# Kernel optimization log

Measured on AMD Instinct MI355X. Metric: run time of the kernel, lower is better.

## Reference

```python
import jax, jax.numpy as jnp
import numpy as np

N = 50000   # nodes
E = 800000  # edges (avg degree 16)
D = 128     # hidden dim (GNN_hidden_dim), heads=1
SLOPE = 0.2  # LeakyReLU negative slope (PyG default)


def _w(k, shape, fan_in):
    return jax.random.normal(k, shape, dtype=jnp.float32) * (1.0 / np.sqrt(fan_in))


def setup_inputs() -> dict:
    key = jax.random.key(0)
    ks = jax.random.split(key, 24)
    inp = {}
    inp["x"] = jax.random.normal(ks[0], (N, D), dtype=jnp.float32)
    inp["edge_index"] = jax.random.randint(ks[1], (2, E), 0, N, dtype=jnp.int32)
    # layer 1 (GATv2 + linear skip)
    inp["Wl1"] = _w(ks[2], (D, D), D); inp["Wr1"] = _w(ks[3], (D, D), D)
    inp["att1"] = _w(ks[4], (D,), D); inp["b1"] = jnp.zeros((D,), jnp.float32)
    inp["Wlin1"] = _w(ks[5], (D, D), D); inp["blin1"] = jnp.zeros((D,), jnp.float32)
    # layer 2
    inp["Wl2"] = _w(ks[6], (D, D), D); inp["Wr2"] = _w(ks[7], (D, D), D)
    inp["att2"] = _w(ks[8], (D,), D); inp["b2"] = jnp.zeros((D,), jnp.float32)
    inp["Wlin2"] = _w(ks[9], (D, D), D); inp["blin2"] = jnp.zeros((D,), jnp.float32)
    # output layer (out_channels=1, heads=1)
    inp["Wlo"] = _w(ks[10], (D, 1), D); inp["Wro"] = _w(ks[11], (D, 1), D)
    inp["atto"] = _w(ks[12], (1,), 1); inp["bo"] = jnp.zeros((1,), jnp.float32)
    inp["Wlino"] = _w(ks[13], (D, 1), D); inp["blino"] = jnp.zeros((1,), jnp.float32)
    return inp


def gatv2(x, src, dst, Wl, Wr, att, b):
    # GATv2 (PyG, add_self_loops=False, share_weights=False, heads=1, no edge_attr)
    xl = x @ Wl            # [N, C] source transform (also message content)
    xr = x @ Wr            # [N, C] target transform
    e = jax.nn.leaky_relu(xl[src] + xr[dst], SLOPE) @ att  # [E] edge logits
    m = jax.ops.segment_max(e, dst, num_segments=N)
    m = jnp.where(jnp.isfinite(m), m, 0.0)  # empty segments
    p = jnp.exp(e - m[dst])
    s = jax.ops.segment_sum(p, dst, num_segments=N)
    alpha = p / (s[dst] + 1e-16)            # segment softmax over incoming edges
    out = jax.ops.segment_sum(alpha[:, None] * xl[src], dst, num_segments=N)
    return out + b


def reference(x, edge_index, Wl1, Wr1, att1, b1, Wlin1, blin1,
              Wl2, Wr2, att2, b2, Wlin2, blin2,
              Wlo, Wro, atto, bo, Wlino, blino):
    src, dst = edge_index[0], edge_index[1]
    h = jax.nn.relu(gatv2(x, src, dst, Wl1, Wr1, att1, b1) + x @ Wlin1 + blin1)
    h = jax.nn.relu(gatv2(h, src, dst, Wl2, Wr2, att2, b2) + h @ Wlin2 + blin2)
    out = gatv2(h, src, dst, Wlo, Wro, atto, bo) + h @ Wlino + blino
    return out  # [N, 1]
```

## Files before the change

kernel.cpp:

```cpp
#include <hip/hip_runtime.h>
#include <hip/hip_bf16.h>
#include <math.h>

#define NN 50000
#define EE 800000
#define DD 128
#define SLOPE 0.2f

typedef __attribute__((ext_vector_type(8))) short short8;
typedef __attribute__((ext_vector_type(4))) float f32x4;

static __device__ __forceinline__ float wred_sum(float v) {
#pragma unroll
    for (int m = 1; m < 64; m <<= 1) v += __shfl_xor(v, m, 64);
    return v;
}

static __device__ __forceinline__ ushort f2bf(float f) {
    __hip_bfloat16 b = __float2bfloat16(f);
    return *reinterpret_cast<ushort*>(&b);
}
static __device__ __forceinline__ float bf2f(unsigned int u) {
    return __uint_as_float((u & 0xffffu) << 16);
}
static __device__ __forceinline__ void unpack8(const uint4& xp, float* xv) {
    xv[0] = bf2f(xp.x); xv[1] = bf2f(xp.x >> 16);
    xv[2] = bf2f(xp.y); xv[3] = bf2f(xp.y >> 16);
    xv[4] = bf2f(xp.z); xv[5] = bf2f(xp.z >> 16);
    xv[6] = bf2f(xp.w); xv[7] = bf2f(xp.w >> 16);
}

__global__ void k_degree(const int* __restrict__ dstv, int* __restrict__ deg,
                         int* __restrict__ epos) {
    int i = blockIdx.x * blockDim.x + threadIdx.x;
    if (i < EE) epos[i] = atomicAdd(&deg[dstv[i]], 1);
}

__global__ void k_blocksum(const int* __restrict__ deg, int* __restrict__ bsum) {
    int t = threadIdx.x;
    int idx = blockIdx.x * 256 + t;
    int v = (idx < NN) ? deg[idx] : 0;
#pragma unroll
    for (int m = 1; m < 64; m <<= 1) v += __shfl_xor(v, m, 64);
    __shared__ int part[4];
    if ((t & 63) == 0) part[t >> 6] = v;
    __syncthreads();
    if (t == 0) bsum[blockIdx.x] = part[0] + part[1] + part[2] + part[3];
}

__global__ void k_scan_bsum(const int* __restrict__ bsum, int* __restrict__ boff, int nb) {
    __shared__ int sd[2][256];
    int t = threadIdx.x;
    int v = (t < nb) ? bsum[t] : 0;
    sd[0][t] = v;
    __syncthreads();
    int s = 0;
    for (int off = 1; off < 256; off <<= 1) {
        int x = sd[s][t];
        if (t >= off) x += sd[s][t - off];
        sd[s ^ 1][t] = x;
        s ^= 1;
        __syncthreads();
    }
    if (t < nb) boff[t] = sd[s][t] - v;
}

__global__ void k_scan_final(const int* __restrict__ deg, const int* __restrict__ boff,
                             int* __restrict__ offs) {
    __shared__ int sd[2][256];
    int t = threadIdx.x;
    int idx = blockIdx.x * 256 + t;
    int v = (idx < NN) ? deg[idx] : 0;
    sd[0][t] = v;
    __syncthreads();
    int s = 0;
    for (int off = 1; off < 256; off <<= 1) {
        int x = sd[s][t];
        if (t >= off) x += sd[s][t - off];
        sd[s ^ 1][t] = x;
        s ^= 1;
        __syncthreads();
    }
    int incl = sd[s][t];
    int base = boff[blockIdx.x];
    if (idx < NN) offs[idx + 1] = base + incl;
    if (idx == 0) offs[0] = 0;
}

__global__ void k_scatter(const int* __restrict__ srcv, const int* __restrict__ dstv,
                          const int* __restrict__ offs, const int* __restrict__ epos,
                          int* __restrict__ csr_src) {
    int i = blockIdx.x * blockDim.x + threadIdx.x;
    if (i < EE) csr_src[offs[dstv[i]] + epos[i]] = srcv[i];
}

__global__ __launch_bounds__(256) void k_wconvert(
    const float* __restrict__ W0, const float* __restrict__ W1, const float* __restrict__ W2,
    const float* __restrict__ W3, const float* __restrict__ W4, const float* __restrict__ W5,
    ushort* __restrict__ Wt) {
    int idx = blockIdx.x * 256 + threadIdx.x;
    int i = idx >> 14;
    int r = idx & 16383;
    int n = r >> 7;
    int k = r & 127;
    const float* Ws[6] = {W0, W1, W2, W3, W4, W5};
    Wt[idx] = f2bf(Ws[i][k * DD + n]);
}

template <int XBF>
__global__ __launch_bounds__(256) void k_gemm3m(
    const float* __restrict__ Xf,
    const ushort* __restrict__ Xb,
    const ushort* __restrict__ Wt,
    ushort* __restrict__ O0b,
    float* __restrict__ O1,
    float* __restrict__ O2) {
    __shared__ ushort wsh[128 * 136];
    int t = threadIdx.x;
    int wid = t >> 6, lane = t & 63;
    int m0 = blockIdx.x * 128 + wid * 32;
    int qrow = lane & 15, kg = lane >> 4;

    short8 afrag[2][4];
#pragma unroll
    for (int mg = 0; mg < 2; mg++) {
#pragma unroll
        for (int ks = 0; ks < 4; ks++) {
            int row = m0 + mg * 16 + qrow;
            row = (row < NN) ? row : (NN - 1);
            if (XBF) {
                afrag[mg][ks] = *reinterpret_cast<const short8*>(
                    Xb + (size_t)row * DD + ks * 32 + kg * 8);
            } else {
                const float* p = Xf + (size_t)row * DD + ks * 32 + kg * 8;
                float4 u0 = *reinterpret_cast<const float4*>(p);
                float4 u1 = *reinterpret_cast<const float4*>(p + 4);
                short8 s;
                s[0] = (short)f2bf(u0.x); s[1] = (short)f2bf(u0.y);
                s[2] = (short)f2bf(u0.z); s[3] = (short)f2bf(u0.w);
                s[4] = (short)f2bf(u1.x); s[5] = (short)f2bf(u1.y);
                s[6] = (short)f2bf(u1.z); s[7] = (short)f2bf(u1.w);
                afrag[mg][ks] = s;
            }
        }
    }

    for (int w = 0; w < 3; w++) {
        __syncthreads();
        const ushort* Wb = Wt + (size_t)w * DD * DD;
#pragma unroll
        for (int i = 0; i < 8; i++) {
            int flat = i * 256 + t;
            int row = flat >> 4, ch = flat & 15;
            short8 v = *reinterpret_cast<const short8*>(Wb + row * DD + ch * 8);
            *reinterpret_cast<short8*>(&wsh[row * 136 + ch * 8]) = v;
        }
        __syncthreads();

        f32x4 acc[2][8];
#pragma unroll
        for (int mg = 0; mg < 2; mg++)
#pragma unroll
            for (int ng = 0; ng < 8; ng++) acc[mg][ng] = (f32x4)(0.f);

#pragma unroll
        for (int ks = 0; ks < 4; ks++) {
            short8 bfrag[8];
#pragma unroll
            for (int ng = 0; ng < 8; ng++)
                bfrag[ng] = *reinterpret_cast<const short8*>(
                    &wsh[(ng * 16 + qrow) * 136 + ks * 32 + kg * 8]);
#pragma unroll
            for (int mg = 0; mg < 2; mg++)
#pragma unroll
                for (int ng = 0; ng < 8; ng++)
                    acc[mg][ng] = __builtin_amdgcn_mfma_f32_16x16x32_bf16(
                        afrag[mg][ks], bfrag[ng], acc[mg][ng], 0, 0, 0);
        }

#pragma unroll
        for (int mg = 0; mg < 2; mg++) {
#pragma unroll
            for (int r = 0; r < 4; r++) {
                int row = m0 + mg * 16 + kg * 4 + r;
                if (row < NN) {
#pragma unroll
                    for (int ng = 0; ng < 8; ng++) {
                        int col = ng * 16 + qrow;
                        float v = acc[mg][ng][r];
                        if (w == 0) O0b[(size_t)row * DD + col] = f2bf(v);
                        else if (w == 1) O1[(size_t)row * DD + col] = v;
                        else O2[(size_t)row * DD + col] = v;
                    }
                }
            }
        }
    }
}

template <int OUTVEC>
__global__ __launch_bounds__(256, 8) void k_fused(
    const int* __restrict__ offs, const int* __restrict__ csr_src,
    const ushort* __restrict__ xlb,
    const float* __restrict__ xr,
    const float* __restrict__ att,
    const float* __restrict__ lin, const float* __restrict__ bb,
    const float* __restrict__ blin, ushort* __restrict__ houtb,
    const float* __restrict__ Wlo, const float* __restrict__ Wro,
    const float* __restrict__ Wlino, const float* __restrict__ blino,
    float* __restrict__ xlo, float* __restrict__ xro, float* __restrict__ lino,
    int nwaves) {
    int gwave = (blockIdx.x * blockDim.x + threadIdx.x) >> 6;
    int lane = threadIdx.x & 63;
    int q = lane >> 4;
    int ql = lane & 15;
    int c0 = ql * 8;

    float av[8];
    {
        float4 a0 = *reinterpret_cast<const float4*>(att + c0);
        float4 a1 = *reinterpret_cast<const float4*>(att + c0 + 4);
        av[0] = a0.x; av[1] = a0.y; av[2] = a0.z; av[3] = a0.w;
        av[4] = a1.x; av[5] = a1.y; av[6] = a1.z; av[7] = a1.w;
    }

    for (int wid = gwave; wid < NN; wid += nwaves) {
        int start = offs[wid];
        int deg = offs[wid + 1] - start;

        float xrv[8];
        {
            float4 t0 = *reinterpret_cast<const float4*>(xr + (size_t)wid * DD + c0);
            float4 t1 = *reinterpret_cast<const float4*>(xr + (size_t)wid * DD + c0 + 4);
            xrv[0] = t0.x; xrv[1] = t0.y; xrv[2] = t0.z; xrv[3] = t0.w;
            xrv[4] = t1.x; xrv[5] = t1.y; xrv[6] = t1.z; xrv[7] = t1.w;
        }

        float ss = 0.f;
        float acc[8];
#pragma unroll
        for (int c = 0; c < 8; c++) acc[c] = 0.f;

        int s_cur = (q < deg) ? csr_src[start + q] : 0;
        uint4 xp = *reinterpret_cast<const uint4*>(xlb + (size_t)s_cur * DD + c0);
        for (int j = q; j < deg; j += 4) {
            int jn = j + 4;
            int s_nxt = (jn < deg) ? csr_src[start + jn] : 0;
            uint4 xpn = *reinterpret_cast<const uint4*>(xlb + (size_t)s_nxt * DD + c0);
            float xv[8];
            unpack8(xp, xv);
            float v = 0.f;
#pragma unroll
            for (int c = 0; c < 8; c++) {
                float u = xv[c] + xrv[c];
                v += fmaxf(u, SLOPE * u) * av[c];
            }
#pragma unroll
            for (int msk = 1; msk < 16; msk <<= 1) v += __shfl_xor(v, msk, 64);
            float p = __expf(v);
            ss += p;
#pragma unroll
            for (int c = 0; c < 8; c++) acc[c] += p * xv[c];
            xp = xpn;
        }

#pragma unroll
        for (int msk = 16; msk < 64; msk <<= 1) {
            ss += __shfl_xor(ss, msk, 64);
#pragma unroll
            for (int c = 0; c < 8; c++) acc[c] += __shfl_xor(acc[c], msk, 64);
        }

        if (q == 0) {
            float inv = 1.f / (ss + 1e-16f);
            float4 l0 = *reinterpret_cast<const float4*>(lin + (size_t)wid * DD + c0);
            float4 l1 = *reinterpret_cast<const float4*>(lin + (size_t)wid * DD + c0 + 4);
            float4 b0 = *reinterpret_cast<const float4*>(bb + c0);
            float4 b1 = *reinterpret_cast<const float4*>(bb + c0 + 4);
            float4 bl0 = *reinterpret_cast<const float4*>(blin + c0);
            float4 bl1 = *reinterpret_cast<const float4*>(blin + c0 + 4);
            float lv[8] = {l0.x, l0.y, l0.z, l0.w, l1.x, l1.y, l1.z, l1.w};
            float bv[8] = {b0.x, b0.y, b0.z, b0.w, b1.x, b1.y, b1.z, b1.w};
            float blv[8] = {bl0.x, bl0.y, bl0.z, bl0.w, bl1.x, bl1.y, bl1.z, bl1.w};
            float o[8];
#pragma unroll
            for (int c = 0; c < 8; c++) o[c] = fmaxf(acc[c] * inv + bv[c] + lv[c] + blv[c], 0.f);

            if (!OUTVEC) {
                uint4 pk;
                pk.x = (unsigned)f2bf(o[0]) | ((unsigned)f2bf(o[1]) << 16);
                pk.y = (unsigned)f2bf(o[2]) | ((unsigned)f2bf(o[3]) << 16);
                pk.z = (unsigned)f2bf(o[4]) | ((unsigned)f2bf(o[5]) << 16);
                pk.w = (unsigned)f2bf(o[6]) | ((unsigned)f2bf(o[7]) << 16);
                *reinterpret_cast<uint4*>(houtb + (size_t)wid * DD + c0) = pk;
            } else {
                float4 w0a = *reinterpret_cast<const float4*>(Wlo + c0);
                float4 w0b = *reinterpret_cast<const float4*>(Wlo + c0 + 4);
                float4 w1a = *reinterpret_cast<const float4*>(Wro + c0);
                float4 w1b = *reinterpret_cast<const float4*>(Wro + c0 + 4);
                float4 w2a = *reinterpret_cast<const float4*>(Wlino + c0);
                float4 w2b = *reinterpret_cast<const float4*>(Wlino + c0 + 4);
                float wv0[8] = {w0a.x, w0a.y, w0a.z, w0a.w, w0b.x, w0b.y, w0b.z, w0b.w};
                float wv1[8] = {w1a.x, w1a.y, w1a.z, w1a.w, w1b.x, w1b.y, w1b.z, w1b.w};
                float wv2[8] = {w2a.x, w2a.y, w2a.z, w2a.w, w2b.x, w2b.y, w2b.z, w2b.w};
                float d0 = 0.f, d1 = 0.f, d2 = 0.f;
#pragma unroll
                for (int c = 0; c < 8; c++) {
                    d0 += o[c] * wv0[c];
                    d1 += o[c] * wv1[c];
                    d2 += o[c] * wv2[c];
                }
#pragma unroll
                for (int msk = 1; msk < 16; msk <<= 1) {
                    d0 += __shfl_xor(d0, msk, 64);
                    d1 += __shfl_xor(d1, msk, 64);
                    d2 += __shfl_xor(d2, msk, 64);
                }
                if (ql == 0) {
                    xlo[wid] = d0;
                    xro[wid] = d1;
                    lino[wid] = d2 + blino[0];
                }
            }
        }
    }
}

__global__ __launch_bounds__(256) void k_aggout(
    const int* __restrict__ offs, const int* __restrict__ csr_src,
    const float* __restrict__ xlo, const float* __restrict__ xro,
    const float* __restrict__ atto, const float* __restrict__ lino,
    const float* __restrict__ bo, float* __restrict__ out) {
    int wid = (blockIdx.x * blockDim.x + threadIdx.x) >> 6;
    int lane = threadIdx.x & 63;
    if (wid >= NN) return;
    int start = offs[wid];
    int deg = offs[wid + 1] - start;
    float xro_w = xro[wid];
    float a0 = atto[0];

    float sl = 0.f, nl = 0.f;
    for (int j = lane; j < deg; j += 64) {
        int s = csr_src[start + j];
        float xs = xlo[s];
        float u = xs + xro_w;
        float e = fmaxf(u, SLOPE * u) * a0;
        float p = __expf(e);
        sl += p;
        nl += p * xs;
    }
    sl = wred_sum(sl);
    nl = wred_sum(nl);
    if (lane == 0) out[wid] = nl / (sl + 1e-16f) + bo[0] + lino[wid];
}

extern "C" void kernel_launch(void* const* d_in, const int* in_sizes, int n_in,
                              void* d_out, int out_size, void* d_ws, size_t ws_size,
                              hipStream_t stream) {
    const float* x = (const float*)d_in[0];
    const int* ei = (const int*)d_in[1];
    const int* srcv = ei;
    const int* dstv = ei + EE;
    const float* Wl1 = (const float*)d_in[2];
    const float* Wr1 = (const float*)d_in[3];
    const float* att1 = (const float*)d_in[4];
    const float* b1 = (const float*)d_in[5];
    const float* Wlin1 = (const float*)d_in[6];
    const float* blin1 = (const float*)d_in[7];
    const float* Wl2 = (const float*)d_in[8];
    const float* Wr2 = (const float*)d_in[9];
    const float* att2 = (const float*)d_in[10];
    const float* b2 = (const float*)d_in[11];
    const float* Wlin2 = (const float*)d_in[12];
    const float* blin2 = (const float*)d_in[13];
    const float* Wlo = (const float*)d_in[14];
    const float* Wro = (const float*)d_in[15];
    const float* atto = (const float*)d_in[16];
    const float* bo = (const float*)d_in[17];
    const float* Wlino = (const float*)d_in[18];
    const float* blino = (const float*)d_in[19];

    char* w = (char*)d_ws;
    auto alloc = [&](size_t bytes) {
        void* p = (void*)w;
        w += (bytes + 255) & ~(size_t)255;
        return p;
    };
    ushort* xlb = (ushort*)alloc((size_t)NN * DD * 2);
    float* xr = (float*)alloc((size_t)NN * DD * 4);
    float* lin = (float*)alloc((size_t)NN * DD * 4);
    ushort* hb = (ushort*)alloc((size_t)NN * DD * 2);
    ushort* Wt = (ushort*)alloc((size_t)6 * DD * DD * 2);
    float* xlo = (float*)alloc((size_t)NN * 4);
    float* xro = (float*)alloc((size_t)NN * 4);
    float* lino = (float*)alloc((size_t)NN * 4);
    int* deg = (int*)alloc((size_t)NN * 4);
    int* offs = (int*)alloc((size_t)(NN + 1) * 4);
    int* bsum = (int*)alloc(256 * 4);
    int* boff = (int*)alloc(256 * 4);
    int* csr_src = (int*)alloc((size_t)(EE + 8) * 4);
    int* epos = (int*)alloc((size_t)EE * 4);

    const int NB = (NN + 255) / 256;

    hipMemsetAsync(deg, 0, (size_t)NN * 4, stream);
    k_degree<<<(EE + 255) / 256, 256, 0, stream>>>(dstv, deg, epos);
    k_blocksum<<<NB, 256, 0, stream>>>(deg, bsum);
    k_scan_bsum<<<1, 256, 0, stream>>>(bsum, boff, NB);
    k_scan_final<<<NB, 256, 0, stream>>>(deg, boff, offs);
    k_scatter<<<(EE + 255) / 256, 256, 0, stream>>>(srcv, dstv, offs, epos, csr_src);

    k_wconvert<<<(6 * DD * DD) / 256, 256, 0, stream>>>(Wl1, Wr1, Wlin1, Wl2, Wr2, Wlin2, Wt);

    const int GEMM_GRID = (NN + 127) / 128;
    const int NODE_GRID = (NN * 64 + 255) / 256;
    const int PERS_BLOCKS = 2048;
    const int PERS_WAVES = PERS_BLOCKS * 4;

    k_gemm3m<0><<<GEMM_GRID, 256, 0, stream>>>(x, nullptr, Wt + (size_t)0 * 3 * DD * DD,
                                               xlb, xr, lin);
    k_fused<0><<<PERS_BLOCKS, 256, 0, stream>>>(offs, csr_src, xlb, xr, att1, lin, b1, blin1, hb,
                                                nullptr, nullptr, nullptr, nullptr,
                                                nullptr, nullptr, nullptr, PERS_WAVES);
    k_gemm3m<1><<<GEMM_GRID, 256, 0, stream>>>(nullptr, hb, Wt + (size_t)1 * 3 * DD * DD,
                                               xlb, xr, lin);
    k_fused<1><<<PERS_BLOCKS, 256, 0, stream>>>(offs, csr_src, xlb, xr, att2, lin, b2, blin2,
                                                nullptr, Wlo, Wro, Wlino, blino,
                                                xlo, xro, lino, PERS_WAVES);
    k_aggout<<<NODE_GRID, 256, 0, stream>>>(offs, csr_src, xlo, xro, atto, lino, bo, (float*)d_out);
}
```

Before: 220.2 us.

## Store xr and skip projections in bf16 and use one wave per node

The GEMM now writes all three projections (xl, xr, linear skip) as bf16 instead of writing xr and lin in fp32, which halves the bytes written and later read for those buffers. The fused aggregation kernel drops the persistent grid-stride loop and the software prefetch of the next neighbour row. It launches one wave per node with default launch bounds instead. The aim is to cut memory traffic and let the hardware scheduler hide gather latency, at the cost of some precision in xr and the skip term and the loss of explicit prefetching.

Result: no change. 223.2 us (+1.4%).

```diff
diff --git a/kernel.cpp b/kernel.cpp
--- a/kernel.cpp
+++ b/kernel.cpp
@@ -113,8 +113,8 @@
     const ushort* __restrict__ Xb,
     const ushort* __restrict__ Wt,
     ushort* __restrict__ O0b,
-    float* __restrict__ O1,
-    float* __restrict__ O2) {
+    ushort* __restrict__ O1b,
+    ushort* __restrict__ O2b) {
     __shared__ ushort wsh[128 * 136];
     int t = threadIdx.x;
     int wid = t >> 6, lane = t & 63;
@@ -178,6 +178,7 @@
                         afrag[mg][ks], bfrag[ng], acc[mg][ng], 0, 0, 0);
         }
 
+        ushort* Ob = (w == 0) ? O0b : (w == 1) ? O1b : O2b;
 #pragma unroll
         for (int mg = 0; mg < 2; mg++) {
 #pragma unroll
@@ -187,10 +188,7 @@
 #pragma unroll
                     for (int ng = 0; ng < 8; ng++) {
                         int col = ng * 16 + qrow;
-                        float v = acc[mg][ng][r];
-                        if (w == 0) O0b[(size_t)row * DD + col] = f2bf(v);
-                        else if (w == 1) O1[(size_t)row * DD + col] = v;
-                        else O2[(size_t)row * DD + col] = v;
+                        Ob[(size_t)row * DD + col] = f2bf(acc[mg][ng][r]);
                     }
                 }
             }
@@ -199,19 +197,20 @@
 }
 
 template <int OUTVEC>
-__global__ __launch_bounds__(256, 8) void k_fused(
+__global__ __launch_bounds__(256) void k_fused(
     const int* __restrict__ offs, const int* __restrict__ csr_src,
     const ushort* __restrict__ xlb,
-    const float* __restrict__ xr,
+    const ushort* __restrict__ xrb,
     const float* __restrict__ att,
-    const float* __restrict__ lin, const float* __restrict__ bb,
+    const ushort* __restrict__ linb,
+    const float* __restrict__ bb,
     const float* __restrict__ blin, ushort* __restrict__ houtb,
     const float* __restrict__ Wlo, const float* __restrict__ Wro,
     const float* __restrict__ Wlino, const float* __restrict__ blino,
-    float* __restrict__ xlo, float* __restrict__ xro, float* __restrict__ lino,
-    int nwaves) {
-    int gwave = (blockIdx.x * blockDim.x + threadIdx.x) >> 6;
+    float* __restrict__ xlo, float* __restrict__ xro, float* __restrict__ lino) {
+    int wid = (blockIdx.x * blockDim.x + threadIdx.x) >> 6;
     int lane = threadIdx.x & 63;
+    if (wid >= NN) return;
     int q = lane >> 4;
     int ql = lane & 15;
     int c0 = ql * 8;
@@ -223,104 +222,97 @@
         av[0] = a0.x; av[1] = a0.y; av[2] = a0.z; av[3] = a0.w;
         av[4] = a1.x; av[5] = a1.y; av[6] = a1.z; av[7] = a1.w;
     }
-
-    for (int wid = gwave; wid < NN; wid += nwaves) {
-        int start = offs[wid];
-        int deg = offs[wid + 1] - start;
-
-        float xrv[8];
+    float xrv[8];
+    {
+        uint4 xrp = *reinterpret_cast<const uint4*>(xrb + (size_t)wid * DD + c0);
+        unpack8(xrp, xrv);
+    }
+
+    int start = offs[wid];
+    int deg = offs[wid + 1] - start;
+
+    float ss = 0.f;
+    float acc[8];
+#pragma unroll
+    for (int c = 0; c < 8; c++) acc[c] = 0.f;
+
+    for (int j = q; j < deg; j += 4) {
+        int s = csr_src[start + j];
+        uint4 xp = *reinterpret_cast<const uint4*>(xlb + (size_t)s * DD + c0);
+        float xv[8];
+        unpack8(xp, xv);
+        float v = 0.f;
+#pragma unroll
+        for (int c = 0; c < 8; c++) {
+            float u = xv[c] + xrv[c];
+            v += fmaxf(u, SLOPE * u) * av[c];
+        }
+#pragma unroll
+        for (int msk = 1; msk < 16; msk <<= 1) v += __shfl_xor(v, msk, 64);
+        float p = __expf(v);
+        ss += p;
+#pragma unroll
+        for (int c = 0; c < 8; c++) acc[c] += p * xv[c];
+    }
+
+#pragma unroll
+    for (int msk = 16; msk < 64; msk <<= 1) {
+        ss += __shfl_xor(ss, msk, 64);
+#pragma unroll
+        for (int c = 0; c < 8; c++) acc[c] += __shfl_xor(acc[c], msk, 64);
+    }
+
+    if (q == 0) {
+        float inv = 1.f / (ss + 1e-16f);
+        float lv[8];
         {
-            float4 t0 = *reinterpret_cast<const float4*>(xr + (size_t)wid * DD + c0);
-            float4 t1 = *reinterpret_cast<const float4*>(xr + (size_t)wid * DD + c0 + 4);
-            xrv[0] = t0.x; xrv[1] = t0.y; xrv[2] = t0.z; xrv[3] = t0.w;
-            xrv[4] = t1.x; xrv[5] = t1.y; xrv[6] = t1.z; xrv[7] = t1.w;
-        }
-
-        float ss = 0.f;
-        float acc[8];
-#pragma unroll
-        for (int c = 0; c < 8; c++) acc[c] = 0.f;
-
-        int s_cur = (q < deg) ? csr_src[start + q] : 0;
-        uint4 xp = *reinterpret_cast<const uint4*>(xlb + (size_t)s_cur * DD + c0);
-        for (int j = q; j < deg; j += 4) {
-            int jn = j + 4;
-            int s_nxt = (jn < deg) ? csr_src[start + jn] : 0;
-            uint4 xpn = *reinterpret_cast<const uint4*>(xlb + (size_t)s_nxt * DD + c0);
-            float xv[8];
-            unpack8(xp, xv);
-            float v = 0.f;
+            uint4 lp = *reinterpret_cast<const uint4*>(linb + (size_t)wid * DD + c0);
+            unpack8(lp, lv);
+        }
+        float4 b0 = *reinterpret_cast<const float4*>(bb + c0);
+        float4 b1 = *reinterpret_cast<const float4*>(bb + c0 + 4);
+        float4 bl0 = *reinterpret_cast<const float4*>(blin + c0);
+        float4 bl1 = *reinterpret_cast<const float4*>(blin + c0 + 4);
+        float bv[8] = {b0.x, b0.y, b0.z, b0.w, b1.x, b1.y, b1.z, b1.w};
+        float blv[8] = {bl0.x, bl0.y, bl0.z, bl0.w, bl1.x, bl1.y, bl1.z, bl1.w};
+        float o[8];
+#pragma unroll
+        for (int c = 0; c < 8; c++) o[c] = fmaxf(acc[c] * inv + bv[c] + lv[c] + blv[c], 0.f);
+
+        if (!OUTVEC) {
+            uint4 pk;
+            pk.x = (unsigned)f2bf(o[0]) | ((unsigned)f2bf(o[1]) << 16);
+            pk.y = (unsigned)f2bf(o[2]) | ((unsigned)f2bf(o[3]) << 16);
+            pk.z = (unsigned)f2bf(o[4]) | ((unsigned)f2bf(o[5]) << 16);
+            pk.w = (unsigned)f2bf(o[6]) | ((unsigned)f2bf(o[7]) << 16);
+            *reinterpret_cast<uint4*>(houtb + (size_t)wid * DD + c0) = pk;
+        } else {
+            float4 w0a = *reinterpret_cast<const float4*>(Wlo + c0);
+            float4 w0b = *reinterpret_cast<const float4*>(Wlo + c0 + 4);
+            float4 w1a = *reinterpret_cast<const float4*>(Wro + c0);
+            float4 w1b = *reinterpret_cast<const float4*>(Wro + c0 + 4);
+            float4 w2a = *reinterpret_cast<const float4*>(Wlino + c0);
+            float4 w2b = *reinterpret_cast<const float4*>(Wlino + c0 + 4);
+            float wv0[8] = {w0a.x, w0a.y, w0a.z, w0a.w, w0b.x, w0b.y, w0b.z, w0b.w};
+            float wv1[8] = {w1a.x, w1a.y, w1a.z, w1a.w, w1b.x, w1b.y, w1b.z, w1b.w};
+            float wv2[8] = {w2a.x, w2a.y, w2a.z, w2a.w, w2b.x, w2b.y, w2b.z, w2b.w};
+            float d0 = 0.f, d1 = 0.f, d2 = 0.f;
 #pragma unroll
             for (int c = 0; c < 8; c++) {
-                float u = xv[c] + xrv[c];
-                v += fmaxf(u, SLOPE * u) * av[c];
+                d0 += o[c] * wv0[c];
+                d1 += o[c] * wv1[c];
+                d2 += o[c] * wv2[c];
             }
 #pragma unroll
-            for (int msk = 1; msk < 16; msk <<= 1) v += __shfl_xor(v, msk, 64);
-            float p = __expf(v);
-            ss += p;
-#pragma unroll
-            for (int c = 0; c < 8; c++) acc[c] += p * xv[c];
-            xp = xpn;
-        }
-
-#pragma unroll
-        for (int msk = 16; msk < 64; msk <<= 1) {
-            ss += __shfl_xor(ss, msk, 64);
-#pragma unroll
-            for (int c = 0; c < 8; c++) acc[c] += __shfl_xor(acc[c], msk, 64);
-        }
-
-        if (q == 0) {
-            float inv = 1.f / (ss + 1e-16f);
-            float4 l0 = *reinterpret_cast<const float4*>(lin + (size_t)wid * DD + c0);
-            float4 l1 = *reinterpret_cast<const float4*>(lin + (size_t)wid * DD + c0 + 4);
-            float4 b0 = *reinterpret_cast<const float4*>(bb + c0);
-            float4 b1 = *reinterpret_cast<const float4*>(bb + c0 + 4);
-            float4 bl0 = *reinterpret_cast<const float4*>(blin + c0);
-            float4 bl1 = *reinterpret_cast<const float4*>(blin + c0 + 4);
-            float lv[8] = {l0.x, l0.y, l0.z, l0.w, l1.x, l1.y, l1.z, l1.w};
-            float bv[8] = {b0.x, b0.y, b0.z, b0.w, b1.x, b1.y, b1.z, b1.w};
-            float blv[8] = {bl0.x, bl0.y, bl0.z, bl0.w, bl1.x, bl1.y, bl1.z, bl1.w};
-            float o[8];
-#pragma unroll
-            for (int c = 0; c < 8; c++) o[c] = fmaxf(acc[c] * inv + bv[c] + lv[c] + blv[c], 0.f);
-
-            if (!OUTVEC) {
-                uint4 pk;
-                pk.x = (unsigned)f2bf(o[0]) | ((unsigned)f2bf(o[1]) << 16);
-                pk.y = (unsigned)f2bf(o[2]) | ((unsigned)f2bf(o[3]) << 16);
-                pk.z = (unsigned)f2bf(o[4]) | ((unsigned)f2bf(o[5]) << 16);
-                pk.w = (unsigned)f2bf(o[6]) | ((unsigned)f2bf(o[7]) << 16);
-                *reinterpret_cast<uint4*>(houtb + (size_t)wid * DD + c0) = pk;
-            } else {
-                float4 w0a = *reinterpret_cast<const float4*>(Wlo + c0);
-                float4 w0b = *reinterpret_cast<const float4*>(Wlo + c0 + 4);
-                float4 w1a = *reinterpret_cast<const float4*>(Wro + c0);
-                float4 w1b = *reinterpret_cast<const float4*>(Wro + c0 + 4);
-                float4 w2a = *reinterpret_cast<const float4*>(Wlino + c0);
-                float4 w2b = *reinterpret_cast<const float4*>(Wlino + c0 + 4);
-                float wv0[8] = {w0a.x, w0a.y, w0a.z, w0a.w, w0b.x, w0b.y, w0b.z, w0b.w};
-                float wv1[8] = {w1a.x, w1a.y, w1a.z, w1a.w, w1b.x, w1b.y, w1b.z, w1b.w};
-                float wv2[8] = {w2a.x, w2a.y, w2a.z, w2a.w, w2b.x, w2b.y, w2b.z, w2b.w};
-                float d0 = 0.f, d1 = 0.f, d2 = 0.f;
-#pragma unroll
-                for (int c = 0; c < 8; c++) {
-                    d0 += o[c] * wv0[c];
-                    d1 += o[c] * wv1[c];
-                    d2 += o[c] * wv2[c];
-                }
-#pragma unroll
-                for (int msk = 1; msk < 16; msk <<= 1) {
-                    d0 += __shfl_xor(d0, msk, 64);
-                    d1 += __shfl_xor(d1, msk, 64);
-                    d2 += __shfl_xor(d2, msk, 64);
-                }
-                if (ql == 0) {
-                    xlo[wid] = d0;
-                    xro[wid] = d1;
-                    lino[wid] = d2 + blino[0];
-                }
+            for (int msk = 1; msk < 16; msk <<= 1) {
+                d0 += __shfl_xor(d0, msk, 64);
+                d1 += __shfl_xor(d1, msk, 64);
+                d2 += __shfl_xor(d2, msk, 64);
+            }
+            if (ql == 0) {
+                xlo[wid] = d0;
+                xro[wid] = d1;
+                lino[wid] = d2 + blino[0];
             }
         }
     }
@@ -387,8 +379,8 @@
         return p;
     };
     ushort* xlb = (ushort*)alloc((size_t)NN * DD * 2);
-    float* xr = (float*)alloc((size_t)NN * DD * 4);
-    float* lin = (float*)alloc((size_t)NN * DD * 4);
+    ushort* xrb = (ushort*)alloc((size_t)NN * DD * 2);
+    ushort* linb = (ushort*)alloc((size_t)NN * DD * 2);
     ushort* hb = (ushort*)alloc((size_t)NN * DD * 2);
     ushort* Wt = (ushort*)alloc((size_t)6 * DD * DD * 2);
     float* xlo = (float*)alloc((size_t)NN * 4);
@@ -398,7 +390,7 @@
     int* offs = (int*)alloc((size_t)(NN + 1) * 4);
     int* bsum = (int*)alloc(256 * 4);
     int* boff = (int*)alloc(256 * 4);
-    int* csr_src = (int*)alloc((size_t)(EE + 8) * 4);
+    int* csr_src = (int*)alloc((size_t)(EE + 16) * 4);
     int* epos = (int*)alloc((size_t)EE * 4);
 
     const int NB = (NN + 255) / 256;
@@ -414,18 +406,16 @@
 
     const int GEMM_GRID = (NN + 127) / 128;
     const int NODE_GRID = (NN * 64 + 255) / 256;
-    const int PERS_BLOCKS = 2048;
-    const int PERS_WAVES = PERS_BLOCKS * 4;
 
     k_gemm3m<0><<<GEMM_GRID, 256, 0, stream>>>(x, nullptr, Wt + (size_t)0 * 3 * DD * DD,
-                                               xlb, xr, lin);
-    k_fused<0><<<PERS_BLOCKS, 256, 0, stream>>>(offs, csr_src, xlb, xr, att1, lin, b1, blin1, hb,
-                                                nullptr, nullptr, nullptr, nullptr,
-                                                nullptr, nullptr, nullptr, PERS_WAVES);
+                                               xlb, xrb, linb);
+    k_fused<0><<<NODE_GRID, 256, 0, stream>>>(offs, csr_src, xlb, xrb, att1, linb, b1, blin1, hb,
+                                              nullptr, nullptr, nullptr, nullptr,
+                                              nullptr, nullptr, nullptr);
     k_gemm3m<1><<<GEMM_GRID, 256, 0, stream>>>(nullptr, hb, Wt + (size_t)1 * 3 * DD * DD,
-                                               xlb, xr, lin);
-    k_fused<1><<<PERS_BLOCKS, 256, 0, stream>>>(offs, csr_src, xlb, xr, att2, lin, b2, blin2,
-                                                nullptr, Wlo, Wro, Wlino, blino,
-                                                xlo, xro, lino, PERS_WAVES);
+                                               xlb, xrb, linb);
+    k_fused<1><<<NODE_GRID, 256, 0, stream>>>(offs, csr_src, xlb, xrb, att2, linb, b2, blin2,
+                                              nullptr, Wlo, Wro, Wlino, blino,
+                                              xlo, xro, lino);
     k_aggout<<<NODE_GRID, 256, 0, stream>>>(offs, csr_src, xlo, xro, atto, lino, bo, (float*)d_out);
 }
```
